# Kernel tuning notes

Measured on AMD Instinct MI355X. Metric: run time of the kernel, lower is better.

The kernel has to match this reference:

```python
import jax, jax.numpy as jnp
import numpy as np

NHEAD = 8
HB, WB = 16, 16  # block_size


def _mha(q, k, v, w_in, b_in, w_out, b_out, nhead):
    # q,k,v: [L, B, C] seq-first, like torch.nn.MultiheadAttention (eval mode, no dropout)
    Lq, B, C = q.shape
    d = C // nhead
    wq, wk, wv = jnp.split(w_in, 3, axis=0)
    bq, bk, bv = jnp.split(b_in, 3)
    qh = (q @ wq.T + bq).reshape(Lq, B, nhead, d).transpose(1, 2, 0, 3)        # [B,H,Lq,d]
    kh = (k @ wk.T + bk).reshape(k.shape[0], B, nhead, d).transpose(1, 2, 0, 3)
    vh = (v @ wv.T + bv).reshape(v.shape[0], B, nhead, d).transpose(1, 2, 0, 3)
    scale = 1.0 / jnp.sqrt(jnp.asarray(d, dtype=qh.dtype))
    scores = jnp.einsum('bhqd,bhkd->bhqk', qh * scale, kh)
    attn = jax.nn.softmax(scores, axis=-1)
    out = jnp.einsum('bhqk,bhkd->bhqd', attn, vh)                               # [B,H,Lq,d]
    out = out.transpose(2, 0, 1, 3).reshape(Lq, B, C)
    return out @ w_out.T + b_out


def setup_inputs() -> dict:
    key = jax.random.key(0)
    ks = jax.random.split(key, 12)
    n, c, t, h, w = 2, 256, 2, 64, 64
    q = jax.random.normal(ks[0], (n, c, t, h, w), dtype=jnp.float32)
    k = jax.random.normal(ks[1], (n, c, t, h, w), dtype=jnp.float32)
    v = jax.random.normal(ks[2], (n, c, t, h, w), dtype=jnp.float32)
    pos = jax.random.normal(ks[3], (n, c, t, h, w), dtype=jnp.float32)
    s = 0.02
    wl_in = jax.random.normal(ks[4], (3 * c, c), dtype=jnp.float32) * s
    bl_in = jnp.zeros((3 * c,), dtype=jnp.float32)
    wl_out = jax.random.normal(ks[5], (c, c), dtype=jnp.float32) * s
    bl_out = jnp.zeros((c,), dtype=jnp.float32)
    ws_in = jax.random.normal(ks[6], (3 * c, c), dtype=jnp.float32) * s
    bs_in = jnp.zeros((3 * c,), dtype=jnp.float32)
    ws_out = jax.random.normal(ks[7], (c, c), dtype=jnp.float32) * s
    bs_out = jnp.zeros((c,), dtype=jnp.float32)
    return {"q": q, "k": k, "v": v, "pos": pos,
            "wl_in": wl_in, "bl_in": bl_in, "wl_out": wl_out, "bl_out": bl_out,
            "ws_in": ws_in, "bs_in": bs_in, "ws_out": ws_out, "bs_out": bs_out}


def reference(q, k, v, pos, wl_in, bl_in, wl_out, bl_out, ws_in, bs_in, ws_out, bs_out):
    n, c, t_q, h, w = q.shape
    t_k = k.shape[2]
    bn_h, bn_w = h // HB, w // WB

    def to_long(x, t):
        # [n,c,t,h,w] -> [t*bn_h*bn_w, n*HB*WB, c]
        x = x.reshape(n, c, t, bn_h, HB, bn_w, WB).transpose(2, 3, 5, 0, 4, 6, 1)
        return x.reshape(t * bn_h * bn_w, n * HB * WB, c)

    ql = to_long(q, t_q)
    kl = to_long(k, t_k)
    vl = to_long(v, t_k)
    pl = to_long(pos, t_q)

    v1 = _mha(ql + pl, kl + pl, vl, wl_in, bl_in, wl_out, bl_out, NHEAD)

    def long_to_short(x):
        # [t*bn_h*bn_w, n*HB*WB, c] -> [t*HB*WB, n*bn_h*bn_w, c]
        x = x.reshape(t_q, bn_h, bn_w, n, HB, WB, c).transpose(0, 4, 5, 3, 1, 2, 6)
        return x.reshape(t_q * HB * WB, n * bn_h * bn_w, c)

    v2 = long_to_short(v1)
    ps = long_to_short(pl)

    out = _mha(v2 + ps, v2 + ps, v2, ws_in, bs_in, ws_out, bs_out, NHEAD)
    out = out.reshape(t_q, HB, WB, n, bn_h, bn_w, c).transpose(3, 6, 0, 4, 1, 5, 2)
    return out.reshape(n, c, t_q, h, w)
```

## Files before the change

### kernel.cpp

```cpp
#include <hip/hip_runtime.h>
#include <math.h>


#define SCALE_D32 0.17677669529663687f
#define EXP2_SCALE 0.25508680987930193f
#define GLOBAL_AS __attribute__((address_space(1)))
#define LDS_AS __attribute__((address_space(3)))

typedef short short8 __attribute__((ext_vector_type(8)));
typedef short short4v __attribute__((ext_vector_type(4)));
typedef short short2v __attribute__((ext_vector_type(2)));
typedef float floatx4 __attribute__((ext_vector_type(4)));

__device__ __forceinline__ short f2bf(float f) {
  union { float f; unsigned u; } x;
  x.f = f;
  unsigned r = x.u + 0x7fffu + ((x.u >> 16) & 1u);
  return (short)(r >> 16);
}
__device__ __forceinline__ float bf2f(short s) {
  union { unsigned u; float f; } x;
  x.u = ((unsigned)(unsigned short)s) << 16;
  return x.f;
}

__device__ __forceinline__ int o1s_phys(int q, int ch) {
  return q * 256 + (ch & ~63) + ((((ch >> 3) & 7) ^ (q & 7)) << 3) + (ch & 7);
}

__device__ __forceinline__ void stage_w(short* Wsl, const short* Wg, int kb,
                                        int wave, int lane, int rsub, int csub) {
#pragma unroll
  for (int j = 0; j < 8; ++j) {
    int r0 = (wave * 8 + j) * 8;
    int row = r0 + rsub;
    int c = csub ^ (row & 7);
    const short* gp = Wg + (long)row * 256 + kb * 64 + c * 8;
    short* lp = &Wsl[r0 * 64 + lane * 8];
    __builtin_amdgcn_global_load_lds((const GLOBAL_AS void*)gp,
                                     (LDS_AS void*)lp, 16, 0, 0);
  }
}

__device__ __forceinline__ void stage_w32(short* buf, const short* Wg,
                                          int kb32, int tid) {
#pragma unroll
  for (int j = 0; j < 4; ++j) {
    int row = j * 64 + (tid >> 2);
    int c = tid & 3;
    int cs = c ^ ((row >> 1) & 3);
    const short* gp = Wg + (long)row * 256 + kb32 * 32 + cs * 8;
    short* lp = buf + j * 2048 + tid * 8;
    __builtin_amdgcn_global_load_lds((const GLOBAL_AS void*)gp,
                                     (LDS_AS void*)lp, 16, 0, 0);
  }
}

__device__ __forceinline__ void gemm32_pipe(
    const short* A, const short* Wg, const short* Wng, bool prestaged,
    short* bufA, short* bufB, floatx4 (&acc)[2][4],
    int tid, int wave, int l15, int quad, int x7) {
  if (!prestaged) {
    stage_w32(bufA, Wg, 0, tid);
    __syncthreads();
  }
  int pcB = quad ^ ((l15 >> 1) & 3);
#pragma unroll
  for (int t = 0; t < 8; ++t) {
    const short* cur = (t & 1) ? bufB : bufA;
    short* nxt = (t & 1) ? bufA : bufB;
    if (t < 7) stage_w32(nxt, Wg, t + 1, tid);
    else if (Wng) stage_w32(nxt, Wng, 0, tid);
    int pcA = ((t & 1) * 4 + quad) ^ x7;
    short8 af[2], bfr[4];
#pragma unroll
    for (int mt = 0; mt < 2; ++mt)
      af[mt] = *(const short8*)&A[(mt * 16 + l15) * 256 + (t >> 1) * 64 + pcA * 8];
#pragma unroll
    for (int nt = 0; nt < 4; ++nt)
      bfr[nt] = *(const short8*)&cur[(wave * 64 + nt * 16 + l15) * 32 + pcB * 8];
#pragma unroll
    for (int mt = 0; mt < 2; ++mt)
#pragma unroll
      for (int nt = 0; nt < 4; ++nt)
        acc[mt][nt] = __builtin_amdgcn_mfma_f32_16x16x32_bf16(
            af[mt], bfr[nt], acc[mt][nt], 0, 0, 0);
    __syncthreads();
  }
}

__device__ __forceinline__ void stage_tile(short* dst, const short* Xg,
                                           int b1, int tid) {
#pragma unroll
  for (int p = 0; p < 4; ++p) {
    int idx = p * 256 + tid;
    int row = idx >> 5;
    int ch = idx & 31;
    int chs = (ch & ~7) | ((ch & 7) ^ (row & 7));
    const short* gp = Xg + ((long)(row * 512 + b1)) * 256 + chs * 8;
    short* lp = dst + idx * 8;
    __builtin_amdgcn_global_load_lds((const GLOBAL_AS void*)gp,
                                     (LDS_AS void*)lp, 16, 0, 0);
  }
}

__global__ __launch_bounds__(256) void pack_kernel(
    const float* __restrict__ q, const float* __restrict__ k,
    const float* __restrict__ v, const float* __restrict__ pos,
    short* __restrict__ Xp, short* __restrict__ Xq,
    short* __restrict__ Xk, short* __restrict__ Xv,
    const float* __restrict__ wl_in, const float* __restrict__ wl_out,
    const float* __restrict__ ws_in, const float* __restrict__ ws_out,
    short* __restrict__ wbf) {
  __shared__ float tP[64][65];
  __shared__ float tX[64][65];
  int b = blockIdx.x;
  int cb = b & 3;
  int h  = (b >> 2) & 63;
  int nt = b >> 8;
  int n = nt >> 1, t = nt & 1;
  int c0 = cb * 64;
  int bh = h >> 4, ii = h & 15;
  long inbase = (long)n * 2097152 + (long)t * 4096 + (long)h * 64;
  int tx = threadIdx.x & 63;
  int ty = threadIdx.x >> 6;

  for (int cc = ty; cc < 64; cc += 4) {
    long a = inbase + (long)(c0 + cc) * 8192 + tx;
    tP[cc][tx] = pos[a];
    tX[cc][tx] = q[a];
  }
  __syncthreads();
  for (int ww = ty; ww < 64; ww += 4) {
    int bw = ww >> 4, j = ww & 15;
    int m1 = (((t * 4 + bh) * 4 + bw) * 512) + n * 256 + ii * 16 + j;
    long o = (long)m1 * 256 + c0 + tx;
    float pv = tP[tx][ww];
    Xp[o] = f2bf(pv);
    Xq[o] = f2bf(tX[tx][ww] + pv);
  }
  __syncthreads();
  for (int cc = ty; cc < 64; cc += 4) {
    long a = inbase + (long)(c0 + cc) * 8192 + tx;
    tX[cc][tx] = k[a];
  }
  __syncthreads();
  for (int ww = ty; ww < 64; ww += 4) {
    int bw = ww >> 4, j = ww & 15;
    int m1 = (((t * 4 + bh) * 4 + bw) * 512) + n * 256 + ii * 16 + j;
    long o = (long)m1 * 256 + c0 + tx;
    Xk[o] = f2bf(tX[tx][ww] + tP[tx][ww]);
  }
  __syncthreads();
  for (int cc = ty; cc < 64; cc += 4) {
    long a = inbase + (long)(c0 + cc) * 8192 + tx;
    tX[cc][tx] = v[a];
  }
  __syncthreads();
  for (int ww = ty; ww < 64; ww += 4) {
    int bw = ww >> 4, j = ww & 15;
    int m1 = (((t * 4 + bh) * 4 + bw) * 512) + n * 256 + ii * 16 + j;
    long o = (long)m1 * 256 + c0 + tx;
    Xv[o] = f2bf(tX[tx][ww]);
  }
  int idx = (blockIdx.x * 256 + threadIdx.x) * 2;
  const float* wp;
  if (idx < 196608) wp = wl_in + idx;
  else if (idx < 262144) wp = wl_out + (idx - 196608);
  else if (idx < 458752) wp = ws_in + (idx - 262144);
  else wp = ws_out + (idx - 458752);
  float2 wv = *(const float2*)wp;
  wbf[idx] = f2bf(wv.x);
  wbf[idx + 1] = f2bf(wv.y);
}

template <bool OUT32>
__global__ __launch_bounds__(256) void gemm_tri(
    const short* __restrict__ A0, const short* __restrict__ A1,
    const short* __restrict__ A2, const short* __restrict__ W0,
    const float* __restrict__ bias0, void* __restrict__ C0,
    void* __restrict__ C1, void* __restrict__ C2) {
  __shared__ short As[128 * 64];
  __shared__ short Ws[64 * 64];
  int z = blockIdx.z;
  const short* A = (z == 0) ? A0 : ((z == 1) ? A1 : A2);
  const short* Wb = W0 + z * 65536;
  const float* bias = bias0 + z * 256;
  void* Csel = (z == 0) ? C0 : ((z == 1) ? C1 : C2);
  int m0 = blockIdx.x * 128;
  int n0 = blockIdx.y * 64;
  int tid = threadIdx.x;
  int lane = tid & 63, wave = tid >> 6;
  int wm = wave >> 1, wn = wave & 1;
  int l15 = lane & 15, quad = lane >> 4;
  int x7 = l15 & 7;
  int rsub = lane >> 3;
  int csub = lane & 7;

  floatx4 acc[4][2];
#pragma unroll
  for (int mt = 0; mt < 4; ++mt)
#pragma unroll
    for (int nt = 0; nt < 2; ++nt) acc[mt][nt] = (floatx4)(0.f);

  for (int kb = 0; kb < 4; ++kb) {
    int k0 = kb * 64;
    if (kb) __syncthreads();
#pragma unroll
    for (int j = 0; j < 4; ++j) {
      int r0 = (wave * 4 + j) * 8;
      int row = r0 + rsub;
      int c = csub ^ (row & 7);
      const short* gp = A + (long)(m0 + row) * 256 + k0 + c * 8;
      short* lp = &As[r0 * 64 + lane * 8];
      __builtin_amdgcn_global_load_lds((const GLOBAL_AS void*)gp,
                                       (LDS_AS void*)lp, 16, 0, 0);
    }
#pragma unroll
    for (int j = 0; j < 2; ++j) {
      int r0 = (wave * 2 + j) * 8;
      int row = r0 + rsub;
      int c = csub ^ (row & 7);
      const short* gp = Wb + (long)(n0 + row) * 256 + k0 + c * 8;
      short* lp = &Ws[r0 * 64 + lane * 8];
      __builtin_amdgcn_global_load_lds((const GLOBAL_AS void*)gp,
                                       (LDS_AS void*)lp, 16, 0, 0);
    }
    __syncthreads();
#pragma unroll
    for (int ks = 0; ks < 2; ++ks) {
      int pc = (ks * 4 + quad) ^ x7;
      short8 af[4], bfr[2];
#pragma unroll
      for (int mt = 0; mt < 4; ++mt) {
        int row = wm * 64 + mt * 16 + l15;
        af[mt] = *(const short8*)&As[row * 64 + pc * 8];
      }
#pragma unroll
      for (int nt = 0; nt < 2; ++nt) {
        int row = wn * 32 + nt * 16 + l15;
        bfr[nt] = *(const short8*)&Ws[row * 64 + pc * 8];
      }
#pragma unroll
      for (int mt = 0; mt < 4; ++mt)
#pragma unroll
        for (int nt = 0; nt < 2; ++nt)
          acc[mt][nt] = __builtin_amdgcn_mfma_f32_16x16x32_bf16(
              af[mt], bfr[nt], acc[mt][nt], 0, 0, 0);
    }
  }
  float bia0 = bias[n0 + wn * 32 + l15];
  float bia1 = bias[n0 + wn * 32 + 16 + l15];
#pragma unroll
  for (int mt = 0; mt < 4; ++mt) {
#pragma unroll
    for (int r = 0; r < 4; ++r) {
      int row = m0 + wm * 64 + mt * 16 + quad * 4 + r;
      long base = (long)row * 256 + n0 + wn * 32 + l15;
      if (OUT32) {
        float* C = (float*)Csel;
        C[base] = acc[mt][0][r] + bia0;
        C[base + 16] = acc[mt][1][r] + bia1;
      } else {
        short* C = (short*)Csel;
        C[base] = f2bf(acc[mt][0][r] + bia0);
        C[base + 16] = f2bf(acc[mt][1][r] + bia1);
      }
    }
  }
}

__global__ __launch_bounds__(256) void attn1_giga(
    const short* __restrict__ Xq, const short* __restrict__ Xk,
    const short* __restrict__ Xv, const short* __restrict__ Xp,
    const short* __restrict__ Wlin, const float* __restrict__ bias_lin,
    const short* __restrict__ Wo, const float* __restrict__ bias_o,
    const short* __restrict__ Wsin, const float* __restrict__ bias_sin,
    short* __restrict__ Q2, short* __restrict__ K2, short* __restrict__ V2) {
  __shared__ short R1[32 * 256];
  __shared__ short R2[32 * 256];
  __shared__ short R3[32 * 256];
  __shared__ short R4[2 * 8192];
  int b1 = blockIdx.x;
  int tid = threadIdx.x;
  int wave = tid >> 6, lane = tid & 63;
  int l15 = lane & 15, quad = lane >> 4;
  int x7 = l15 & 7;

  short* bufA = R4;
  short* bufB = R4 + 8192;

  stage_tile(R1, Xq, b1, tid);
  stage_tile(R2, Xk, b1, tid);
  stage_tile(R3, Xv, b1, tid);

  floatx4 acc[2][4];

#pragma unroll 1
  for (int z = 0; z < 3; ++z) {
    short* Rz = (z == 0) ? R1 : ((z == 1) ? R2 : R3);
    const short* Wz = Wlin + z * 65536;
    const short* Wn = (z < 2) ? (Wlin + (z + 1) * 65536) : (const short*)0;
#pragma unroll
    for (int mt = 0; mt < 2; ++mt)
#pragma unroll
      for (int nt = 0; nt < 4; ++nt) acc[mt][nt] = (floatx4)(0.f);
    gemm32_pipe(Rz, Wz, Wn, z > 0, bufA, bufB, acc, tid, wave, l15, quad, x7);
    float bz[4];
#pragma unroll
    for (int nt = 0; nt < 4; ++nt)
      bz[nt] = bias_lin[z * 256 + wave * 64 + nt * 16 + l15];
#pragma unroll
    for (int mt = 0; mt < 2; ++mt)
#pragma unroll
      for (int r = 0; r < 4; ++r) {
        int row = mt * 16 + quad * 4 + r;
#pragma unroll
        for (int nt = 0; nt < 4; ++nt) {
          int col = wave * 64 + nt * 16 + l15;
          Rz[o1s_phys(row, col)] = f2bf(acc[mt][nt][r] + bz[nt]);
        }
      }
  }
  __syncthreads();

  short* Vtb = R4;
  short* Pwb = R4 + 5120;
  int key = lane & 31;
  int dh = (lane >> 5) * 16;
  int pc2 = 2 * (key & 15) + (key >> 4);

  floatx4 oacc[2][4];
  float lsum[2][2][4];

#pragma unroll
  for (int h2 = 0; h2 < 2; ++h2) {
    int hh = wave * 2 + h2;
    int cb0 = hh * 32 + quad * 8;
    short8 qf0 = *(const short8*)&R1[o1s_phys(l15, cb0)];
    short8 qf1 = *(const short8*)&R1[o1s_phys(l15 + 16, cb0)];
    short8 kf0 = *(const short8*)&R2[o1s_phys(l15, cb0)];
    short8 kf1 = *(const short8*)&R2[o1s_phys(l15 + 16, cb0)];
    short8 v0 = *(const short8*)&R3[o1s_phys(key, hh * 32 + dh)];
    short8 v1 = *(const short8*)&R3[o1s_phys(key, hh * 32 + dh + 8)];
#pragma unroll
    for (int j = 0; j < 8; ++j) {
      Vtb[(wave * 32 + dh + j) * 40 + pc2] = v0[j];
      Vtb[(wave * 32 + dh + 8 + j) * 40 + pc2] = v1[j];
    }
    floatx4 s00 = __builtin_amdgcn_mfma_f32_16x16x32_bf16(qf0, kf0, (floatx4)(0.f), 0, 0, 0);
    floatx4 s01 = __builtin_amdgcn_mfma_f32_16x16x32_bf16(qf0, kf1, (floatx4)(0.f), 0, 0, 0);
    floatx4 s10 = __builtin_amdgcn_mfma_f32_16x16x32_bf16(qf1, kf0, (floatx4)(0.f), 0, 0, 0);
    floatx4 s11 = __builtin_amdgcn_mfma_f32_16x16x32_bf16(qf1, kf1, (floatx4)(0.f), 0, 0, 0);
    float li0[4], li1[4];
#pragma unroll
    for (int r = 0; r < 4; ++r) {
      float p00 = __builtin_amdgcn_exp2f(s00[r] * EXP2_SCALE);
      float p01 = __builtin_amdgcn_exp2f(s01[r] * EXP2_SCALE);
      float p10 = __builtin_amdgcn_exp2f(s10[r] * EXP2_SCALE);
      float p11 = __builtin_amdgcn_exp2f(s11[r] * EXP2_SCALE);
      li0[r] = p00 + p01;
      li1[r] = p10 + p11;
      short2v pa, pb;
      pa.x = f2bf(p00); pa.y = f2bf(p01);
      pb.x = f2bf(p10); pb.y = f2bf(p11);
      *(short2v*)&Pwb[(wave * 32 + quad * 4 + r) * 40 + 2 * l15] = pa;
      *(short2v*)&Pwb[(wave * 32 + 16 + quad * 4 + r) * 40 + 2 * l15] = pb;
    }
#pragma unroll
    for (int r = 0; r < 4; ++r) {
      li0[r] += __shfl_xor(li0[r], 1, 64);
      li0[r] += __shfl_xor(li0[r], 2, 64);
      li0[r] += __shfl_xor(li0[r], 4, 64);
      li0[r] += __shfl_xor(li0[r], 8, 64);
      li1[r] += __shfl_xor(li1[r], 1, 64);
      li1[r] += __shfl_xor(li1[r], 2, 64);
      li1[r] += __shfl_xor(li1[r], 4, 64);
      li1[r] += __shfl_xor(li1[r], 8, 64);
      lsum[h2][0][r] = li0[r];
      lsum[h2][1][r] = li1[r];
    }
    short8 pf0 = *(const short8*)&Pwb[(wave * 32 + l15) * 40 + quad * 8];
    short8 pf1 = *(const short8*)&Pwb[(wave * 32 + 16 + l15) * 40 + quad * 8];
    short8 vt0 = *(const short8*)&Vtb[(wave * 32 + l15) * 40 + quad * 8];
    short8 vt1 = *(const short8*)&Vtb[(wave * 32 + 16 + l15) * 40 + quad * 8];
    oacc[h2][0] = __builtin_amdgcn_mfma_f32_16x16x32_bf16(pf0, vt0, (floatx4)(0.f), 0, 0, 0);
    oacc[h2][1] = __builtin_amdgcn_mfma_f32_16x16x32_bf16(pf0, vt1, (floatx4)(0.f), 0, 0, 0);
    oacc[h2][2] = __builtin_amdgcn_mfma_f32_16x16x32_bf16(pf1, vt0, (floatx4)(0.f), 0, 0, 0);
    oacc[h2][3] = __builtin_amdgcn_mfma_f32_16x16x32_bf16(pf1, vt1, (floatx4)(0.f), 0, 0, 0);
  }

  __syncthreads();

  stage_w32(bufA, Wo, 0, tid);
#pragma unroll
  for (int h2 = 0; h2 < 2; ++h2) {
    int hh = wave * 2 + h2;
    int cA = hh * 32 + l15;
    int cB = cA + 16;
#pragma unroll
    for (int r = 0; r < 4; ++r) {
      float inv0 = 1.f / lsum[h2][0][r];
      float inv1 = 1.f / lsum[h2][1][r];
      int qa = quad * 4 + r, qb = 16 + quad * 4 + r;
      R1[o1s_phys(qa, cA)] = f2bf(oacc[h2][0][r] * inv0);
      R1[o1s_phys(qa, cB)] = f2bf(oacc[h2][1][r] * inv0);
      R1[o1s_phys(qb, cA)] = f2bf(oacc[h2][2][r] * inv1);
      R1[o1s_phys(qb, cB)] = f2bf(oacc[h2][3][r] * inv1);
    }
  }
  __syncthreads();

#pragma unroll
  for (int mt = 0; mt < 2; ++mt)
#pragma unroll
    for (int nt = 0; nt < 4; ++nt) acc[mt][nt] = (floatx4)(0.f);
  gemm32_pipe(R1, Wo, Wsin, true, bufA, bufB, acc, tid, wave, l15, quad, x7);

  {
    float bvo[4];
#pragma unroll
    for (int nt = 0; nt < 4; ++nt) bvo[nt] = bias_o[wave * 64 + nt * 16 + l15];
#pragma unroll
    for (int mt = 0; mt < 2; ++mt) {
#pragma unroll
      for (int r = 0; r < 4; ++r) {
        int qrow = mt * 16 + quad * 4 + r;
        long pbase = ((long)qrow * 512 + b1) * 256;
#pragma unroll
        for (int nt = 0; nt < 4; ++nt) {
          int col = wave * 64 + nt * 16 + l15;
          float val = acc[mt][nt][r] + bvo[nt];
          int ph = o1s_phys(qrow, col);
          R3[ph] = f2bf(val);
          R2[ph] = f2bf(val + bf2f(Xp[pbase + col]));
        }
      }
    }
  }
  __syncthreads();

  int nn = b1 >> 8, ii = (b1 >> 4) & 15, jj = b1 & 15;
#pragma unroll 1
  for (int z = 0; z < 3; ++z) {
    const short* Wz = Wsin + z * 65536;
    const short* Wn = (z < 2) ? (Wsin + (z + 1) * 65536) : (const short*)0;
    const short* Ab = (z < 2) ? R2 : R3;
    short* outz = (z == 0) ? Q2 : ((z == 1) ? K2 : V2);
    float bz[4];
#pragma unroll
    for (int nt = 0; nt < 4; ++nt)
      bz[nt] = bias_sin[z * 256 + wave * 64 + nt * 16 + l15];
#pragma unroll
    for (int mt = 0; mt < 2; ++mt)
#pragma unroll
      for (int nt = 0; nt < 4; ++nt) acc[mt][nt] = (floatx4)(0.f);
    gemm32_pipe(Ab, Wz, Wn, true, bufA, bufB, acc, tid, wave, l15, quad, x7);
#pragma unroll
    for (int mt = 0; mt < 2; ++mt) {
#pragma unroll
      for (int r = 0; r < 4; ++r) {
        int qrow = mt * 16 + quad * 4 + r;
        int t = qrow >> 4, bh = (qrow >> 2) & 3, bw = qrow & 3;
        int m2 = (t * 256 + ii * 16 + jj) * 32 + nn * 16 + bh * 4 + bw;
        long xbase = (long)m2 * 256;
#pragma unroll
        for (int nt = 0; nt < 4; ++nt) {
          int col = wave * 64 + nt * 16 + l15;
          outz[xbase + col] = f2bf(acc[mt][nt][r] + bz[nt]);
        }
      }
    }
  }
}

__global__ __launch_bounds__(256) void attn2_mfma(
    const short* __restrict__ Q2, const short* __restrict__ K2,
    const short* __restrict__ V2, short* __restrict__ O2) {
  __shared__ short Ks[64][40];
  __shared__ short Vt[32][72];
  __shared__ short Pw[4][16][72];
  int bid = blockIdx.x;
  int rest = bid & 255;
  int qblk = bid >> 8;
  int hh = 2 * (rest & 3) + (rest >> 7);
  int b2 = (rest >> 2) & 31;
  int tid = threadIdx.x;
  int wave = tid >> 6, lane = tid & 63;
  int l15 = lane & 15, quad = lane >> 4;

  short8 qf;
  {
    long tok = (long)(qblk * 64 + wave * 16 + l15) * 32 + b2;
    qf = *(const short8*)(Q2 + tok * 256 + hh * 32 + quad * 8);
  }
  floatx4 Oa = (floatx4)(0.f), Ob = (floatx4)(0.f);
  float li[4] = {0.f, 0.f, 0.f, 0.f};

  int skey = tid >> 2;
  int sd0 = (tid & 3) * 8;
  int vkey = lane;
  int vd0 = wave * 8;
  int vcol = (vkey & 15) * 4 + (vkey >> 4);

  for (int kb = 0; kb < 8; ++kb) {
    if (kb) __syncthreads();
    {
      long tok = (long)(kb * 64 + skey) * 32 + b2;
      *(short8*)&Ks[skey][sd0] = *(const short8*)(K2 + tok * 256 + hh * 32 + sd0);
    }
    {
      long tok = (long)(kb * 64 + vkey) * 32 + b2;
      short8 v = *(const short8*)(V2 + tok * 256 + hh * 32 + vd0);
#pragma unroll
      for (int j = 0; j < 8; ++j) Vt[vd0 + j][vcol] = v[j];
    }
    __syncthreads();
    floatx4 st[4];
#pragma unroll
    for (int kt = 0; kt < 4; ++kt) {
      short8 kf = *(const short8*)&Ks[kt * 16 + l15][quad * 8];
      st[kt] = __builtin_amdgcn_mfma_f32_16x16x32_bf16(qf, kf, (floatx4)(0.f), 0, 0, 0);
    }
#pragma unroll
    for (int r = 0; r < 4; ++r) {
      float p0 = __builtin_amdgcn_exp2f(st[0][r] * EXP2_SCALE);
      float p1 = __builtin_amdgcn_exp2f(st[1][r] * EXP2_SCALE);
      float p2 = __builtin_amdgcn_exp2f(st[2][r] * EXP2_SCALE);
      float p3 = __builtin_amdgcn_exp2f(st[3][r] * EXP2_SCALE);
      li[r] += (p0 + p1) + (p2 + p3);
      short4v pp;
      pp.x = f2bf(p0); pp.y = f2bf(p1); pp.z = f2bf(p2); pp.w = f2bf(p3);
      *(short4v*)&Pw[wave][quad * 4 + r][l15 * 4] = pp;
    }
#pragma unroll
    for (int kk = 0; kk < 2; ++kk) {
      short8 pf = *(const short8*)&Pw[wave][l15][kk * 32 + quad * 8];
      short8 v0 = *(const short8*)&Vt[l15][kk * 32 + quad * 8];
      short8 v1 = *(const short8*)&Vt[16 + l15][kk * 32 + quad * 8];
      Oa = __builtin_amdgcn_mfma_f32_16x16x32_bf16(pf, v0, Oa, 0, 0, 0);
      Ob = __builtin_amdgcn_mfma_f32_16x16x32_bf16(pf, v1, Ob, 0, 0, 0);
    }
  }
#pragma unroll
  for (int r = 0; r < 4; ++r) {
    float s = li[r];
    s += __shfl_xor(s, 1, 64);
    s += __shfl_xor(s, 2, 64);
    s += __shfl_xor(s, 4, 64);
    s += __shfl_xor(s, 8, 64);
    float inv = 1.f / s;
    long tok = (long)(qblk * 64 + wave * 16 + quad * 4 + r) * 32 + b2;
    long a = tok * 256 + hh * 32 + l15;
    O2[a] = f2bf(Oa[r] * inv);
    O2[a + 16] = f2bf(Ob[r] * inv);
  }
}

__global__ __launch_bounds__(256) void unpack_kernel(
    const float* __restrict__ Y, float* __restrict__ out) {
  __shared__ float tl[64][65];
  int b = blockIdx.x;
  int cb = b & 3;
  int h = (b >> 2) & 63;
  int nt = b >> 8;
  int n = nt >> 1, t = nt & 1;
  int c0 = cb * 64;
  int bh = h >> 4, ii = h & 15;
  int tx = threadIdx.x & 63;
  int ty = threadIdx.x >> 6;
  for (int ww = ty; ww < 64; ww += 4) {
    int bw = ww >> 4, j = ww & 15;
    int l2 = t * 256 + ii * 16 + j;
    int b2 = n * 16 + bh * 4 + bw;
    int m2 = l2 * 32 + b2;
    tl[tx][ww] = Y[(long)m2 * 256 + c0 + tx];
  }
  __syncthreads();
  long ob = (long)n * 2097152 + (long)t * 4096 + (long)h * 64 + tx;
  for (int cc = ty; cc < 64; cc += 4) {
    out[ob + (long)(c0 + cc) * 8192] = tl[cc][tx];
  }
}

extern "C" void kernel_launch(void* const* d_in, const int* in_sizes, int n_in,
                              void* d_out, int out_size, void* d_ws, size_t ws_size,
                              hipStream_t stream) {
  const float* q      = (const float*)d_in[0];
  const float* k      = (const float*)d_in[1];
  const float* v      = (const float*)d_in[2];
  const float* pos    = (const float*)d_in[3];
  const float* wl_in  = (const float*)d_in[4];
  const float* bl_in  = (const float*)d_in[5];
  const float* wl_out = (const float*)d_in[6];
  const float* bl_out = (const float*)d_in[7];
  const float* ws_in  = (const float*)d_in[8];
  const float* bs_in  = (const float*)d_in[9];
  const float* ws_out = (const float*)d_in[10];
  const float* bs_out = (const float*)d_in[11];
  float* out = (float*)d_out;
  char* wsb = (char*)d_ws;
  const size_t SLB = 16777216;
  short* s0 = (short*)(wsb);
  short* wbf = (short*)(wsb + SLB / 2);
  short* s1 = (short*)(wsb + SLB);
  short* s2 = (short*)(wsb + 2 * SLB);
  short* s3 = (short*)(wsb + 3 * SLB);
  short* s4 = (short*)(wsb + 4 * SLB);
  short* s5 = (short*)(wsb + 5 * SLB);
  short* s6 = (short*)(wsb + 6 * SLB);

  pack_kernel<<<1024, 256, 0, stream>>>(q, k, v, pos, s0, s1, s2, s3,
                                        wl_in, wl_out, ws_in, ws_out, wbf);

  attn1_giga<<<512, 256, 0, stream>>>(s1, s2, s3, s0, wbf, bl_in,
                                      wbf + 196608, bl_out,
                                      wbf + 262144, bs_in, s4, s5, s6);

  attn2_mfma<<<2048, 256, 0, stream>>>(s4, s5, s6, s1);
  dim3 g1(128, 4, 1);
  gemm_tri<true><<<g1, 256, 0, stream>>>(s1, s1, s1, wbf + 458752, bs_out,
                                         s2, s2, s2);

  unpack_kernel<<<1024, 256, 0, stream>>>((const float*)s2, out);
}
```

Baseline: 207.6 us.

## Load weight fragments directly from global into registers instead of LDS staging

Replaces the LDS double-buffered weight staging in the fused attention kernel's GEMMs with direct global-to-register loads of B fragments, prefetched one k-step ahead. This removes the per-k-step __syncthreads barriers and shrinks LDS use (R4 goes from 16384 to 10240 shorts), which may allow more blocks per CU. In exchange each wave issues its own uncoalesced 16-byte global loads of weight rows, relying on L2/L1 caching, with less latency hiding than the asynchronous LDS pipeline. Explicit barriers are added after the tile staging and after each first-stage GEMM to keep LDS reuse correct.

```diff
diff --git a/kernel.cpp b/kernel.cpp
--- a/kernel.cpp
+++ b/kernel.cpp
@@ -42,50 +42,36 @@
   }
 }
 
-__device__ __forceinline__ void stage_w32(short* buf, const short* Wg,
-                                          int kb32, int tid) {
-#pragma unroll
-  for (int j = 0; j < 4; ++j) {
-    int row = j * 64 + (tid >> 2);
-    int c = tid & 3;
-    int cs = c ^ ((row >> 1) & 3);
-    const short* gp = Wg + (long)row * 256 + kb32 * 32 + cs * 8;
-    short* lp = buf + j * 2048 + tid * 8;
-    __builtin_amdgcn_global_load_lds((const GLOBAL_AS void*)gp,
-                                     (LDS_AS void*)lp, 16, 0, 0);
-  }
-}
-
-__device__ __forceinline__ void gemm32_pipe(
-    const short* A, const short* Wg, const short* Wng, bool prestaged,
-    short* bufA, short* bufB, floatx4 (&acc)[2][4],
-    int tid, int wave, int l15, int quad, int x7) {
-  if (!prestaged) {
-    stage_w32(bufA, Wg, 0, tid);
-    __syncthreads();
-  }
-  int pcB = quad ^ ((l15 >> 1) & 3);
+__device__ __forceinline__ void gemm_direct(
+    const short* A, const short* Wg, floatx4 (&acc)[2][4],
+    int wave, int l15, int quad, int x7) {
+  const short* wrow = Wg + (wave * 64 + l15) * 256 + quad * 8;
+  short8 bcur[4], bnxt[4];
+#pragma unroll
+  for (int nt = 0; nt < 4; ++nt)
+    bcur[nt] = *(const short8*)(wrow + nt * 16 * 256);
 #pragma unroll
   for (int t = 0; t < 8; ++t) {
-    const short* cur = (t & 1) ? bufB : bufA;
-    short* nxt = (t & 1) ? bufA : bufB;
-    if (t < 7) stage_w32(nxt, Wg, t + 1, tid);
-    else if (Wng) stage_w32(nxt, Wng, 0, tid);
+    if (t < 7) {
+#pragma unroll
+      for (int nt = 0; nt < 4; ++nt)
+        bnxt[nt] = *(const short8*)(wrow + nt * 16 * 256 + (t + 1) * 32);
+    }
     int pcA = ((t & 1) * 4 + quad) ^ x7;
-    short8 af[2], bfr[4];
+    short8 af[2];
 #pragma unroll
     for (int mt = 0; mt < 2; ++mt)
       af[mt] = *(const short8*)&A[(mt * 16 + l15) * 256 + (t >> 1) * 64 + pcA * 8];
 #pragma unroll
-    for (int nt = 0; nt < 4; ++nt)
-      bfr[nt] = *(const short8*)&cur[(wave * 64 + nt * 16 + l15) * 32 + pcB * 8];
-#pragma unroll
     for (int mt = 0; mt < 2; ++mt)
 #pragma unroll
       for (int nt = 0; nt < 4; ++nt)
         acc[mt][nt] = __builtin_amdgcn_mfma_f32_16x16x32_bf16(
-            af[mt], bfr[nt], acc[mt][nt], 0, 0, 0);
-    __syncthreads();
+            af[mt], bcur[nt], acc[mt][nt], 0, 0, 0);
+    if (t < 7) {
+#pragma unroll
+      for (int nt = 0; nt < 4; ++nt) bcur[nt] = bnxt[nt];
+    }
   }
 }
 
@@ -280,19 +266,17 @@
   __shared__ short R1[32 * 256];
   __shared__ short R2[32 * 256];
   __shared__ short R3[32 * 256];
-  __shared__ short R4[2 * 8192];
+  __shared__ short R4[10240];
   int b1 = blockIdx.x;
   int tid = threadIdx.x;
   int wave = tid >> 6, lane = tid & 63;
   int l15 = lane & 15, quad = lane >> 4;
   int x7 = l15 & 7;
 
-  short* bufA = R4;
-  short* bufB = R4 + 8192;
-
   stage_tile(R1, Xq, b1, tid);
   stage_tile(R2, Xk, b1, tid);
   stage_tile(R3, Xv, b1, tid);
+  __syncthreads();
 
   floatx4 acc[2][4];
 
@@ -300,12 +284,12 @@
   for (int z = 0; z < 3; ++z) {
     short* Rz = (z == 0) ? R1 : ((z == 1) ? R2 : R3);
     const short* Wz = Wlin + z * 65536;
-    const short* Wn = (z < 2) ? (Wlin + (z + 1) * 65536) : (const short*)0;
 #pragma unroll
     for (int mt = 0; mt < 2; ++mt)
 #pragma unroll
       for (int nt = 0; nt < 4; ++nt) acc[mt][nt] = (floatx4)(0.f);
-    gemm32_pipe(Rz, Wz, Wn, z > 0, bufA, bufB, acc, tid, wave, l15, quad, x7);
+    gemm_direct(Rz, Wz, acc, wave, l15, quad, x7);
+    __syncthreads();
     float bz[4];
 #pragma unroll
     for (int nt = 0; nt < 4; ++nt)
@@ -392,7 +376,6 @@
 
   __syncthreads();
 
-  stage_w32(bufA, Wo, 0, tid);
 #pragma unroll
   for (int h2 = 0; h2 < 2; ++h2) {
     int hh = wave * 2 + h2;
@@ -415,7 +398,7 @@
   for (int mt = 0; mt < 2; ++mt)
 #pragma unroll
     for (int nt = 0; nt < 4; ++nt) acc[mt][nt] = (floatx4)(0.f);
-  gemm32_pipe(R1, Wo, Wsin, true, bufA, bufB, acc, tid, wave, l15, quad, x7);
+  gemm_direct(R1, Wo, acc, wave, l15, quad, x7);
 
   {
     float bvo[4];
@@ -444,7 +427,6 @@
 #pragma unroll 1
   for (int z = 0; z < 3; ++z) {
     const short* Wz = Wsin + z * 65536;
-    const short* Wn = (z < 2) ? (Wsin + (z + 1) * 65536) : (const short*)0;
     const short* Ab = (z < 2) ? R2 : R3;
     short* outz = (z == 0) ? Q2 : ((z == 1) ? K2 : V2);
     float bz[4];
@@ -455,7 +437,7 @@
     for (int mt = 0; mt < 2; ++mt)
 #pragma unroll
       for (int nt = 0; nt < 4; ++nt) acc[mt][nt] = (floatx4)(0.f);
-    gemm32_pipe(Ab, Wz, Wn, true, bufA, bufB, acc, tid, wave, l15, quad, x7);
+    gemm_direct(Ab, Wz, acc, wave, l15, quad, x7);
 #pragma unroll
     for (int mt = 0; mt < 2; ++mt) {
 #pragma unroll
```

After: 223.4 us. 7.6% more time.
